# Kernel optimization log

Measured on AMD Instinct MI355X. Metric: run time of the kernel, lower is better.

The kernel has to match this reference:

```python
import jax, jax.numpy as jnp
from jax import lax
import numpy as np

DIM = 256
D_STATE = 16
D_CONV = 4
EXPAND = 2
D_INNER = EXPAND * DIM          # 512
DT_RANK = (DIM + 15) // 16      # 16
EPS = 1e-5


def setup_inputs() -> dict:
    key = jax.random.key(0)
    ks = jax.random.split(key, 8)
    B, H, W = 8, 32, 32
    dt_init = 0.01  # softplus(b_dt) ~= dt_init at init (mamba-style)
    return {
        "x": jax.random.normal(ks[0], (B, DIM, H, W), jnp.float32),
        "ln_gamma": jnp.ones((DIM,), jnp.float32),
        "ln_beta": jnp.zeros((DIM,), jnp.float32),
        "W_in": jax.random.normal(ks[1], (DIM, 2 * D_INNER), jnp.float32) * 0.02,
        "conv_w": jax.random.normal(ks[2], (D_INNER, D_CONV), jnp.float32) * 0.2,
        "conv_b": jnp.zeros((D_INNER,), jnp.float32),
        "W_xproj": jax.random.normal(ks[3], (D_INNER, DT_RANK + 2 * D_STATE), jnp.float32) * 0.02,
        "W_dt": jax.random.normal(ks[4], (DT_RANK, D_INNER), jnp.float32) * 0.05,
        "b_dt": jnp.full((D_INNER,), float(np.log(np.expm1(dt_init))), jnp.float32),
        "A_log": jnp.log(jnp.broadcast_to(
            jnp.arange(1, D_STATE + 1, dtype=jnp.float32), (D_INNER, D_STATE))),
        "D_skip": jnp.ones((D_INNER,), jnp.float32),
        "W_out": jax.random.normal(ks[5], (D_INNER, DIM), jnp.float32) * 0.02,
    }


def _mamba_layer(x, ln_gamma, ln_beta, W_in, conv_w, conv_b, W_xproj,
                 W_dt, b_dt, A_log, D_skip, W_out):
    B, C, H, W = x.shape
    L = H * W
    # (B,C,H,W) -> (B, L, C)
    xf = x.transpose(0, 2, 3, 1).reshape(B, L, C)
    # LayerNorm over channel dim
    mu = xf.mean(-1, keepdims=True)
    var = ((xf - mu) ** 2).mean(-1, keepdims=True)
    xn = (xf - mu) * lax.rsqrt(var + EPS) * ln_gamma + ln_beta
    # in_proj -> u (ssm branch) and z (gate branch)
    xz = xn @ W_in                              # [B, L, 2*D_INNER]
    u, z = xz[..., :D_INNER], xz[..., D_INNER:]
    # causal depthwise conv1d over L, then SiLU
    uc = u.transpose(0, 2, 1)                   # [B, D_INNER, L]
    uc = lax.conv_general_dilated(
        uc, conv_w[:, None, :], window_strides=(1,),
        padding=[(D_CONV - 1, 0)], feature_group_count=D_INNER)
    u2 = jax.nn.silu(uc + conv_b[None, :, None]).transpose(0, 2, 1)  # [B, L, D_INNER]
    # input-dependent dt, B, C
    dbc = u2 @ W_xproj                          # [B, L, DT_RANK + 2*D_STATE]
    dt = jax.nn.softplus(dbc[..., :DT_RANK] @ W_dt + b_dt)            # [B, L, D_INNER]
    Bm = dbc[..., DT_RANK:DT_RANK + D_STATE]    # [B, L, D_STATE]
    Cm = dbc[..., DT_RANK + D_STATE:]           # [B, L, D_STATE]
    A = -jnp.exp(A_log)                         # [D_INNER, D_STATE]

    def step(h, ins):
        dt_t, B_t, C_t, u_t = ins               # [B,Din], [B,S], [B,S], [B,Din]
        dA = jnp.exp(dt_t[:, :, None] * A)      # [B, Din, S]
        h = dA * h + dt_t[:, :, None] * B_t[:, None, :] * u_t[:, :, None]
        y = jnp.einsum('bds,bs->bd', h, C_t)
        return h, y

    h0 = jnp.zeros((B, D_INNER, D_STATE), xf.dtype)
    xs = (dt.transpose(1, 0, 2), Bm.transpose(1, 0, 2),
          Cm.transpose(1, 0, 2), u2.transpose(1, 0, 2))
    _, ys = lax.scan(step, h0, xs)              # ys: [L, B, D_INNER]
    y = ys.transpose(1, 0, 2) + u2 * D_skip     # skip connection D*u
    y = y * jax.nn.silu(z)                      # gate
    o = y @ W_out                               # [B, L, C]
    return o.reshape(B, H, W, C).transpose(0, 3, 1, 2) + x


def reference(x, ln_gamma, ln_beta, W_in, conv_w, conv_b, W_xproj,
              W_dt, b_dt, A_log, D_skip, W_out):
    return _mamba_layer(x, ln_gamma, ln_beta, W_in, conv_w, conv_b, W_xproj,
                        W_dt, b_dt, A_log, D_skip, W_out)
```

## Files before the change

kernel.cpp:

```cpp
#include <hip/hip_runtime.h>
#include <hip/hip_bf16.h>
#include <math.h>

#define DIMC   256
#define DI     512
#define DS     16
#define DTR    16
#define NX     48
#define BATCH  8
#define LSEQ   1024
#define MROWS  8192
#define CHUNK  32
#define NC     (LSEQ / CHUNK)

typedef __attribute__((ext_vector_type(8))) short short8;
typedef __attribute__((ext_vector_type(4))) float f32x4;

__device__ __forceinline__ unsigned short f2bf(float v) {
  __hip_bfloat16 h = __float2bfloat16(v);
  return *reinterpret_cast<unsigned short*>(&h);
}
__device__ __forceinline__ float bf2f(unsigned short u) {
  return __int_as_float(((int)u) << 16);
}

__device__ __forceinline__ void load_lds16(const void* g, void* l) {
  __builtin_amdgcn_global_load_lds(
      (const __attribute__((address_space(1))) unsigned int*)g,
      (__attribute__((address_space(3))) unsigned int*)l, 16, 0, 0);
}

__global__ __launch_bounds__(256) void prologue(const float* __restrict__ W_in,
                                                const float* __restrict__ W_out,
                                                const float* __restrict__ W_xproj,
                                                const float* __restrict__ W_dt,
                                                const float* __restrict__ x,
                                                const float* __restrict__ gamma,
                                                const float* __restrict__ beta,
                                                unsigned short* __restrict__ Wib,
                                                unsigned short* __restrict__ Wob,
                                                unsigned short* __restrict__ Wxpb,
                                                unsigned short* __restrict__ Wdtb,
                                                unsigned short* __restrict__ xnb) {
  __shared__ float sx[DIMC][67];
  __shared__ float smean[64], srs[64];
  const int blk = blockIdx.x, tid = threadIdx.x;
  if (blk < 384) {
    float (*t)[67] = sx;
    const float* W; unsigned short* Wt; int K, N, bx, by;
    if (blk < 256) { W = W_in;  Wt = Wib; K = DIMC; N = 1024; bx = blk & 31; by = blk >> 5; }
    else           { W = W_out; Wt = Wob; K = DI;   N = DIMC; bx = (blk - 256) & 7; by = (blk - 256) >> 3; }
    int n0 = bx * 32, k0 = by * 32;
    int tx = tid & 31, ty = tid >> 5;
    for (int i = ty; i < 32; i += 8) t[i][tx] = W[(size_t)(k0 + i) * N + n0 + tx];
    __syncthreads();
    for (int i = ty; i < 32; i += 8)
      Wt[(size_t)(n0 + i) * K + k0 + tx] = f2bf(t[tx][i]);
    return;
  }
  if (blk < 512) {
    int idx = (blk - 384) * 256 + tid;
    int n = idx >> 9, k = idx & 511;
    Wxpb[idx] = (n < NX) ? f2bf(W_xproj[(size_t)k * NX + n]) : (unsigned short)0;
    return;
  }
  if (blk < 576) {
    int idx = (blk - 512) * 256 + tid;
    int n = idx >> 5, k = idx & 31;
    Wdtb[idx] = (k < DTR) ? f2bf(W_dt[(size_t)k * DI + n]) : (unsigned short)0;
    return;
  }
  const int lb = blk - 576;
  const int b = lb >> 4, l0 = (lb & 15) * 64;
  {
    const int cbase = tid >> 2;
    const int lp = (tid & 3) * 16;
#pragma unroll
    for (int cg = 0; cg < 4; ++cg) {
      const int c = cg * 64 + cbase;
      const float* p = x + ((size_t)b * DIMC + c) * LSEQ + l0 + lp;
#pragma unroll
      for (int q = 0; q < 4; ++q) {
        float4 v = *(const float4*)(p + q * 4);
        sx[c][lp + q * 4 + 0] = v.x;
        sx[c][lp + q * 4 + 1] = v.y;
        sx[c][lp + q * 4 + 2] = v.z;
        sx[c][lp + q * 4 + 3] = v.w;
      }
    }
  }
  __syncthreads();
  {
    const int lane = tid & 63, w = tid >> 6;
    const int l = (w << 4) + (lane & 15);
    const int quad = lane >> 4;
    float sum = 0.f, sq = 0.f;
#pragma unroll 8
    for (int cc = 0; cc < 64; ++cc) {
      float v = sx[quad * 64 + cc][l];
      sum += v; sq += v * v;
    }
    sum += __shfl_xor(sum, 16); sq += __shfl_xor(sq, 16);
    sum += __shfl_xor(sum, 32); sq += __shfl_xor(sq, 32);
    if (quad == 0) {
      float mean = sum * (1.f / 256.f);
      float var  = sq * (1.f / 256.f) - mean * mean;
      smean[l] = mean; srs[l] = rsqrtf(var + 1e-5f);
    }
  }
  __syncthreads();
  {
    const float gg = gamma[tid], bb = beta[tid];
    const size_t base = ((size_t)b * LSEQ + l0) * DIMC + tid;
#pragma unroll 4
    for (int ll = 0; ll < 64; ++ll) {
      float v = (sx[tid][ll] - smean[ll]) * srs[ll] * gg + bb;
      xnb[base + (size_t)ll * DIMC] = f2bf(v);
    }
  }
}

__global__ __launch_bounds__(256) void gemm_bf16_128(const unsigned short* __restrict__ A,
                                                     const unsigned short* __restrict__ Bt,
                                                     unsigned short* __restrict__ Cb,
                                                     int M, int N, int K) {
  __shared__ unsigned short As[128][32];
  __shared__ unsigned short Bs[128][32];
  const int tid = threadIdx.x;
  const int lane = tid & 63, wave = tid >> 6;
  const int wm = wave >> 1, wn = wave & 1;
  const int quad = lane >> 4, l16 = lane & 15;
  const int m0 = blockIdx.y * 128, n0 = blockIdx.x * 128;

  f32x4 acc[4][4];
#pragma unroll
  for (int i = 0; i < 4; ++i)
#pragma unroll
    for (int j = 0; j < 4; ++j) acc[i][j] = (f32x4){0.f, 0.f, 0.f, 0.f};

  for (int k0 = 0; k0 < K; k0 += 32) {
#pragma unroll
    for (int q = 0; q < 2; ++q) {
      int id = q * 256 + tid;
      int row = id >> 2, c = id & 3;
      load_lds16(A + (size_t)(m0 + row) * K + k0 + c * 8,
                 (char*)&As[0][0] + (size_t)(q * 256 + wave * 64) * 16);
    }
#pragma unroll
    for (int q = 0; q < 2; ++q) {
      int id = q * 256 + tid;
      int row = id >> 2, c = id & 3;
      load_lds16(Bt + (size_t)(n0 + row) * K + k0 + c * 8,
                 (char*)&Bs[0][0] + (size_t)(q * 256 + wave * 64) * 16);
    }
    __syncthreads();
    short8 af[4], bfr[4];
#pragma unroll
    for (int i = 0; i < 4; ++i)
      af[i] = *(const short8*)&As[wm * 64 + i * 16 + l16][quad * 8];
#pragma unroll
    for (int j = 0; j < 4; ++j)
      bfr[j] = *(const short8*)&Bs[wn * 64 + j * 16 + l16][quad * 8];
#pragma unroll
    for (int i = 0; i < 4; ++i)
#pragma unroll
      for (int j = 0; j < 4; ++j)
        acc[i][j] = __builtin_amdgcn_mfma_f32_16x16x32_bf16(af[i], bfr[j], acc[i][j], 0, 0, 0);
    __syncthreads();
  }

#pragma unroll
  for (int i = 0; i < 4; ++i) {
    int rowb = wm * 64 + i * 16 + quad * 4;
#pragma unroll
    for (int j = 0; j < 4; ++j) {
      int n = n0 + wn * 64 + j * 16 + l16;
#pragma unroll
      for (int r = 0; r < 4; ++r)
        Cb[(size_t)(m0 + rowb + r) * N + n] = f2bf(acc[i][j][r]);
    }
  }
}

#define GTM 128
#define GTN 64
#define GBK 32
__global__ __launch_bounds__(256) void gemm_bf16(const unsigned short* __restrict__ A,
                                                 const unsigned short* __restrict__ Bt,
                                                 void* __restrict__ Cout,
                                                 int M, int N, int K, int mode,
                                                 const float* __restrict__ X) {
  __shared__ unsigned short As[GTM][GBK];
  __shared__ unsigned short Bs[GTN][GBK];
  const int tid = threadIdx.x;
  const int lane = tid & 63, wave = tid >> 6;
  const int wm = wave >> 1, wn = wave & 1;
  const int quad = lane >> 4, l16 = lane & 15;
  const int m0 = blockIdx.y * GTM, n0 = blockIdx.x * GTN;

  f32x4 acc[4][2];
#pragma unroll
  for (int i = 0; i < 4; ++i)
#pragma unroll
    for (int j = 0; j < 2; ++j) acc[i][j] = (f32x4){0.f, 0.f, 0.f, 0.f};

  for (int k0 = 0; k0 < K; k0 += GBK) {
#pragma unroll
    for (int q = 0; q < 2; ++q) {
      int id = q * 256 + tid;
      int row = id >> 2, c = id & 3;
      load_lds16(A + (size_t)(m0 + row) * K + k0 + c * 8,
                 (char*)&As[0][0] + (size_t)(q * 256 + wave * 64) * 16);
    }
    {
      int row = tid >> 2, c = tid & 3;
      load_lds16(Bt + (size_t)(n0 + row) * K + k0 + c * 8,
                 (char*)&Bs[0][0] + (size_t)(wave * 64) * 16);
    }
    __syncthreads();
    short8 af[4], bfrag[2];
#pragma unroll
    for (int i = 0; i < 4; ++i)
      af[i] = *(const short8*)&As[wm * 64 + i * 16 + l16][quad * 8];
#pragma unroll
    for (int j = 0; j < 2; ++j)
      bfrag[j] = *(const short8*)&Bs[wn * 32 + j * 16 + l16][quad * 8];
#pragma unroll
    for (int i = 0; i < 4; ++i)
#pragma unroll
      for (int j = 0; j < 2; ++j)
        acc[i][j] = __builtin_amdgcn_mfma_f32_16x16x32_bf16(af[i], bfrag[j], acc[i][j], 0, 0, 0);
    __syncthreads();
  }

  if (mode == 2) {
    unsigned short* Cb = (unsigned short*)Cout;
#pragma unroll
    for (int i = 0; i < 4; ++i) {
      int rowb = wm * 64 + i * 16 + quad * 4;
#pragma unroll
      for (int j = 0; j < 2; ++j) {
        int n = n0 + wn * 32 + j * 16 + l16;
#pragma unroll
        for (int r = 0; r < 4; ++r)
          Cb[(size_t)(m0 + rowb + r) * N + n] = f2bf(acc[i][j][r]);
      }
    }
  } else {
    float* C = (float*)Cout;
#pragma unroll
    for (int i = 0; i < 4; ++i) {
      int m = m0 + wm * 64 + i * 16 + quad * 4;
      int b = m >> 10, l = m & 1023;
#pragma unroll
      for (int j = 0; j < 2; ++j) {
        int n = n0 + wn * 32 + j * 16 + l16;
        size_t o = (size_t)b * (DIMC * LSEQ) + (size_t)n * LSEQ + l;
        f32x4 xv = *(const f32x4*)(X + o);
        f32x4 rv = acc[i][j] + xv;
        *(f32x4*)(C + o) = rv;
      }
    }
  }
}

__global__ __launch_bounds__(256) void conv_xproj_dt(
    const unsigned short* __restrict__ xzb,
    const float* __restrict__ conv_w,
    const float* __restrict__ conv_b,
    const unsigned short* __restrict__ Wxpb,
    const unsigned short* __restrict__ Wdtb,
    const float* __restrict__ b_dt,
    float* __restrict__ dbcBC,
    unsigned int* __restrict__ dtu) {
  __shared__ unsigned short sxz[19][512];
  __shared__ unsigned short su[16][512 + 8];
  __shared__ unsigned short sdbc[16][40];
  const int m0 = blockIdx.x * 16;
  const int l0 = m0 & 1023;
  const int tid = threadIdx.x, lane = tid & 63, w = tid >> 6;
  const int quad = lane >> 4, l16 = lane & 15;

#pragma unroll
  for (int q = 0; q < 5; ++q) {
    int id = q * 256 + tid;
    if (id < 19 * 64) {
      int rr = id >> 6, c8 = id & 63;
      uint4 v; v.x = 0u; v.y = 0u; v.z = 0u; v.w = 0u;
      if (l0 - 3 + rr >= 0)
        v = *(const uint4*)(xzb + (size_t)(m0 - 3 + rr) * 1024 + c8 * 8);
      *(uint4*)&sxz[rr][c8 * 8] = v;
    }
  }
  __syncthreads();

#pragma unroll 4
  for (int q = 0; q < 32; ++q) {
    int idx = q * 256 + tid;
    int r = idx >> 9, c = idx & 511;
    float4 wv = *(const float4*)(conv_w + c * 4);
    float acc = conv_b[c];
    acc = fmaf(bf2f(sxz[r + 0][c]), wv.x, acc);
    acc = fmaf(bf2f(sxz[r + 1][c]), wv.y, acc);
    acc = fmaf(bf2f(sxz[r + 2][c]), wv.z, acc);
    acc = fmaf(bf2f(sxz[r + 3][c]), wv.w, acc);
    float u = acc / (1.f + __expf(-acc));
    su[r][c] = f2bf(u);
  }
  __syncthreads();

  f32x4 acc = (f32x4){0.f, 0.f, 0.f, 0.f};
#pragma unroll 4
  for (int k0 = 0; k0 < 512; k0 += 32) {
    short8 af = *(const short8*)&su[l16][k0 + quad * 8];
    short8 bf = *(const short8*)(Wxpb + (size_t)(w * 16 + l16) * 512 + k0 + quad * 8);
    acc = __builtin_amdgcn_mfma_f32_16x16x32_bf16(af, bf, acc, 0, 0, 0);
  }
  if (w == 1 || w == 2) {
#pragma unroll
    for (int r = 0; r < 4; ++r)
      dbcBC[(size_t)(m0 + quad * 4 + r) * 32 + (w - 1) * 16 + l16] = acc[r];
  }
  if (w < 2) {
#pragma unroll
    for (int r = 0; r < 4; ++r)
      sdbc[quad * 4 + r][w * 16 + l16] = f2bf(acc[r]);
  }
  __syncthreads();

  short8 af0 = *(const short8*)&sdbc[l16][quad * 8];
#pragma unroll
  for (int jn = 0; jn < 8; ++jn) {
    const int n0 = w * 128 + jn * 16;
    short8 bf = *(const short8*)(Wdtb + (size_t)(n0 + l16) * 32 + quad * 8);
    f32x4 a0 = (f32x4){0.f, 0.f, 0.f, 0.f};
    a0 = __builtin_amdgcn_mfma_f32_16x16x32_bf16(af0, bf, a0, 0, 0, 0);
    const float bd = b_dt[n0 + l16];
#pragma unroll
    for (int r = 0; r < 4; ++r) {
      int lr0 = quad * 4 + r;
      float v = a0[r] + bd;
      float sp = (v > 20.f) ? v : log1pf(__expf(v));
      unsigned int u0 = (unsigned int)su[lr0][n0 + l16];
      dtu[(size_t)(m0 + lr0) * DI + n0 + l16] = u0 | ((unsigned int)f2bf(sp) << 16);
    }
  }
}

__global__ __launch_bounds__(256) void scan_pass1(const unsigned int* __restrict__ dtu,
                                                  const float* __restrict__ dbcBC,
                                                  const float* __restrict__ A_log,
                                                  float* __restrict__ hend,
                                                  float* __restrict__ Ssum) {
  const int bb = blockIdx.x, dh = blockIdx.y, cc = blockIdx.z;
  const int tid = threadIdx.x;
  const int d = dh * 256 + tid;

  __shared__ float sB[CHUNK][16];
  const size_t mbase = (size_t)bb * LSEQ + cc * CHUNK;
#pragma unroll
  for (int q = 0; q < 2; ++q) {
    int lin = q * 256 + tid;
    int tt = lin >> 4, ss = lin & 15;
    sB[tt][ss] = dbcBC[(mbase + tt) * 32 + ss];
  }

  float Ads[16];
  {
    const f32x4* pa = (const f32x4*)(A_log + (size_t)d * DS);
#pragma unroll
    for (int q = 0; q < 4; ++q) {
      f32x4 v = pa[q];
#pragma unroll
      for (int r = 0; r < 4; ++r) Ads[q * 4 + r] = -__expf(v[r]);
    }
  }
  __syncthreads();

  float h[16];
#pragma unroll
  for (int s = 0; s < 16; ++s) h[s] = 0.f;
  float dts = 0.f;
  const unsigned int* pdu = dtu + mbase * DI + d;
#pragma unroll 4
  for (int tt = 0; tt < CHUNK; ++tt) {
    unsigned int wv = pdu[(size_t)tt * DI];
    float dt = bf2f((unsigned short)(wv >> 16));
    float u  = bf2f((unsigned short)(wv & 0xffff));
    dts += dt;
    float c = dt * u;
#pragma unroll
    for (int s = 0; s < 16; ++s)
      h[s] = fmaf(__expf(dt * Ads[s]), h[s], c * sB[tt][s]);
  }
  const size_t ci = (size_t)(bb * NC + cc) * DI + d;
  f32x4* ph = (f32x4*)(hend + ci * DS);
#pragma unroll
  for (int q = 0; q < 4; ++q) {
    f32x4 v;
#pragma unroll
    for (int r = 0; r < 4; ++r) v[r] = h[q * 4 + r];
    ph[q] = v;
  }
  Ssum[ci] = dts;
}

__global__ __launch_bounds__(256) void scan_pass2(const float* __restrict__ A_log,
                                                  const float* __restrict__ hend,
                                                  const float* __restrict__ Ssum,
                                                  float* __restrict__ hin) {
  const int bb = blockIdx.x, dblk = blockIdx.y;
  const int tid = threadIdx.x;
  const int di = tid >> 4, s = tid & 15;
  const int d = dblk * 16 + di;
  const float Ads = -__expf(A_log[d * DS + s]);
  float h = 0.f;
#pragma unroll 4
  for (int cc = 0; cc < NC; ++cc) {
    size_t ci = ((size_t)(bb * NC + cc) * DI + d);
    hin[ci * DS + s] = h;
    h = fmaf(__expf(Ads * Ssum[ci]), h, hend[ci * DS + s]);
  }
}

__global__ __launch_bounds__(256) void scan_pass3(const unsigned int* __restrict__ dtu,
                                                  const float* __restrict__ dbcBC,
                                                  const unsigned short* __restrict__ xzb,
                                                  const float* __restrict__ A_log,
                                                  const float* __restrict__ D_skip,
                                                  const float* __restrict__ hin,
                                                  unsigned short* __restrict__ yb) {
  const int bb = blockIdx.x, dh = blockIdx.y, cc = blockIdx.z;
  const int tid = threadIdx.x;
  const int d = dh * 256 + tid;

  __shared__ float sB[CHUNK][16];
  __shared__ float sC[CHUNK][16];
  const size_t mbase = (size_t)bb * LSEQ + cc * CHUNK;
#pragma unroll
  for (int q = 0; q < 2; ++q) {
    int lin = q * 256 + tid;
    int tt = lin >> 4, ss = lin & 15;
    sB[tt][ss] = dbcBC[(mbase + tt) * 32 + ss];
    sC[tt][ss] = dbcBC[(mbase + tt) * 32 + 16 + ss];
  }

  float Ads[16];
  {
    const f32x4* pa = (const f32x4*)(A_log + (size_t)d * DS);
#pragma unroll
    for (int q = 0; q < 4; ++q) {
      f32x4 v = pa[q];
#pragma unroll
      for (int r = 0; r < 4; ++r) Ads[q * 4 + r] = -__expf(v[r]);
    }
  }

  float h[16];
  {
    const f32x4* ph = (const f32x4*)(hin + ((size_t)(bb * NC + cc) * DI + d) * DS);
#pragma unroll
    for (int q = 0; q < 4; ++q) {
      f32x4 v = ph[q];
#pragma unroll
      for (int r = 0; r < 4; ++r) h[q * 4 + r] = v[r];
    }
  }
  __syncthreads();

  const float Dsk = D_skip[d];
  const unsigned int* pdu = dtu + mbase * DI + d;
  const unsigned short* pz = xzb + mbase * 1024 + DI + d;
  unsigned short* py = yb + mbase * DI + d;
#pragma unroll 4
  for (int tt = 0; tt < CHUNK; ++tt) {
    unsigned int wv = pdu[(size_t)tt * DI];
    float dt = bf2f((unsigned short)(wv >> 16));
    float u  = bf2f((unsigned short)(wv & 0xffff));
    float c = dt * u;
    float y = u * Dsk;
#pragma unroll
    for (int s = 0; s < 16; ++s) {
      h[s] = fmaf(__expf(dt * Ads[s]), h[s], c * sB[tt][s]);
      y = fmaf(h[s], sC[tt][s], y);
    }
    float z = bf2f(pz[(size_t)tt * 1024]);
    y *= z / (1.f + __expf(-z));
    py[(size_t)tt * DI] = f2bf(y);
  }
}

extern "C" void kernel_launch(void* const* d_in, const int* in_sizes, int n_in,
                              void* d_out, int out_size, void* d_ws, size_t ws_size,
                              hipStream_t stream) {
  const float* x       = (const float*)d_in[0];
  const float* ln_g    = (const float*)d_in[1];
  const float* ln_b    = (const float*)d_in[2];
  const float* W_in    = (const float*)d_in[3];
  const float* conv_w  = (const float*)d_in[4];
  const float* conv_b  = (const float*)d_in[5];
  const float* W_xproj = (const float*)d_in[6];
  const float* W_dt    = (const float*)d_in[7];
  const float* b_dt    = (const float*)d_in[8];
  const float* A_log   = (const float*)d_in[9];
  const float* D_skip  = (const float*)d_in[10];
  const float* W_out   = (const float*)d_in[11];
  float* out = (float*)d_out;

  float* ws    = (float*)d_ws;
  float* dbcBC = ws;
  float* hend  = dbcBC + (size_t)MROWS * 32;
  float* hin   = hend + (size_t)BATCH * NC * DI * DS;
  float* Ssum  = hin  + (size_t)BATCH * NC * DI * DS;
  unsigned int* dtu = (unsigned int*)(Ssum + (size_t)BATCH * NC * DI);
  unsigned short* xzb  = (unsigned short*)(dtu + (size_t)MROWS * DI);
  unsigned short* yb   = xzb + (size_t)MROWS * 1024;
  unsigned short* xnb  = yb;
  unsigned short* Wib  = yb  + (size_t)MROWS * DI;
  unsigned short* Wob  = Wib + (size_t)DIMC * 1024;
  unsigned short* Wxpb = Wob + (size_t)DI * DIMC;
  unsigned short* Wdtb = Wxpb + (size_t)64 * 512;

  prologue<<<704, 256, 0, stream>>>(W_in, W_out, W_xproj, W_dt, x, ln_g, ln_b,
                                    Wib, Wob, Wxpb, Wdtb, xnb);

  gemm_bf16_128<<<dim3(1024 / 128, MROWS / 128), 256, 0, stream>>>(
      xnb, Wib, xzb, MROWS, 1024, DIMC);

  conv_xproj_dt<<<MROWS / 16, 256, 0, stream>>>(xzb, conv_w, conv_b,
                                                Wxpb, Wdtb, b_dt, dbcBC, dtu);

  dim3 gp13(BATCH, 2, NC);
  dim3 gp2(BATCH, DI / 16);
  scan_pass1<<<gp13, 256, 0, stream>>>(dtu, dbcBC, A_log, hend, Ssum);
  scan_pass2<<<gp2, 256, 0, stream>>>(A_log, hend, Ssum, hin);
  scan_pass3<<<gp13, 256, 0, stream>>>(dtu, dbcBC, xzb, A_log, D_skip, hin, yb);

  gemm_bf16<<<dim3(DIMC / GTN, MROWS / GTM), 256, 0, stream>>>(
      yb, Wob, out, MROWS, DIMC, DI, 1, x);
}
```

Measured before the change: 185.9 us.

## Fuse three scan passes into one persistent kernel with grid barriers

Merges the chunked scan's three kernels into a single launch of 512 blocks. Blocks synchronise across the grid with atomic-counter barriers; the counters are reset by the preceding conv kernel. The chunk's dt/u and B/C data are staged once into LDS with async global-to-LDS loads and reused in both the local pass and the output pass, instead of being re-read from global memory. The intent is to remove two launch gaps and the duplicate loads, at the cost of relying on all blocks being co-resident (launch_bounds of 2 blocks per CU) and of spin-wait overhead.

```diff
diff --git a/kernel.cpp b/kernel.cpp
--- a/kernel.cpp
+++ b/kernel.cpp
@@ -28,6 +28,21 @@
   __builtin_amdgcn_global_load_lds(
       (const __attribute__((address_space(1))) unsigned int*)g,
       (__attribute__((address_space(3))) unsigned int*)l, 16, 0, 0);
+}
+
+__device__ __forceinline__ void gridbar(unsigned int* ctr, unsigned int nblk) {
+  __syncthreads();
+  if (threadIdx.x == 0) {
+    __threadfence();
+    __hip_atomic_fetch_add(ctr, 1u, __ATOMIC_ACQ_REL, __HIP_MEMORY_SCOPE_AGENT);
+    for (int it = 0; it < (1 << 20); ++it) {
+      if (__hip_atomic_load(ctr, __ATOMIC_ACQUIRE, __HIP_MEMORY_SCOPE_AGENT) >= nblk)
+        break;
+      __builtin_amdgcn_s_sleep(8);
+    }
+    __threadfence();
+  }
+  __syncthreads();
 }
 
 __global__ __launch_bounds__(256) void prologue(const float* __restrict__ W_in,
@@ -272,7 +287,8 @@
     const unsigned short* __restrict__ Wdtb,
     const float* __restrict__ b_dt,
     float* __restrict__ dbcBC,
-    unsigned int* __restrict__ dtu) {
+    unsigned int* __restrict__ dtu,
+    unsigned int* __restrict__ bar) {
   __shared__ unsigned short sxz[19][512];
   __shared__ unsigned short su[16][512 + 8];
   __shared__ unsigned short sdbc[16][40];
@@ -280,6 +296,8 @@
   const int l0 = m0 & 1023;
   const int tid = threadIdx.x, lane = tid & 63, w = tid >> 6;
   const int quad = lane >> 4, l16 = lane & 15;
+
+  if (blockIdx.x == 0 && tid < 2) bar[tid] = 0u;
 
 #pragma unroll
   for (int q = 0; q < 5; ++q) {
@@ -347,23 +365,36 @@
   }
 }
 
-__global__ __launch_bounds__(256) void scan_pass1(const unsigned int* __restrict__ dtu,
-                                                  const float* __restrict__ dbcBC,
-                                                  const float* __restrict__ A_log,
-                                                  float* __restrict__ hend,
-                                                  float* __restrict__ Ssum) {
+__global__ __launch_bounds__(256, 2) void scan_all(
+    const unsigned int* __restrict__ dtu,
+    const float* __restrict__ dbcBC,
+    const unsigned short* __restrict__ xzb,
+    const float* __restrict__ A_log,
+    const float* __restrict__ D_skip,
+    float* __restrict__ hend,
+    float* __restrict__ Ssum,
+    float* __restrict__ hin,
+    unsigned int* __restrict__ bar,
+    unsigned short* __restrict__ yb) {
   const int bb = blockIdx.x, dh = blockIdx.y, cc = blockIdx.z;
   const int tid = threadIdx.x;
+  const int wave = tid >> 6;
   const int d = dh * 256 + tid;
-
-  __shared__ float sB[CHUNK][16];
+  const unsigned int nblk = gridDim.x * gridDim.y * gridDim.z;
+
+  __shared__ unsigned int sdu[CHUNK][256];
+  __shared__ float sBC[CHUNK][32];
+
   const size_t mbase = (size_t)bb * LSEQ + cc * CHUNK;
-#pragma unroll
-  for (int q = 0; q < 2; ++q) {
-    int lin = q * 256 + tid;
-    int tt = lin >> 4, ss = lin & 15;
-    sB[tt][ss] = dbcBC[(mbase + tt) * 32 + ss];
-  }
+
+#pragma unroll
+  for (int q = 0; q < 8; ++q) {
+    int c = q * 256 + tid;
+    load_lds16(dtu + (mbase + (c >> 6)) * DI + dh * 256 + (c & 63) * 4,
+               (char*)&sdu[0][0] + (size_t)(q * 256 + wave * 64) * 16);
+  }
+  load_lds16(dbcBC + (mbase + (tid >> 3)) * 32 + (tid & 7) * 4,
+             (char*)&sBC[0][0] + (size_t)(wave * 64) * 16);
 
   float Ads[16];
   {
@@ -381,84 +412,59 @@
 #pragma unroll
   for (int s = 0; s < 16; ++s) h[s] = 0.f;
   float dts = 0.f;
-  const unsigned int* pdu = dtu + mbase * DI + d;
 #pragma unroll 4
   for (int tt = 0; tt < CHUNK; ++tt) {
-    unsigned int wv = pdu[(size_t)tt * DI];
+    unsigned int wv = sdu[tt][tid];
     float dt = bf2f((unsigned short)(wv >> 16));
     float u  = bf2f((unsigned short)(wv & 0xffff));
     dts += dt;
-    float c = dt * u;
-#pragma unroll
-    for (int s = 0; s < 16; ++s)
-      h[s] = fmaf(__expf(dt * Ads[s]), h[s], c * sB[tt][s]);
+    float cdu = dt * u;
+    f32x4 B0 = *(const f32x4*)&sBC[tt][0];
+    f32x4 B1 = *(const f32x4*)&sBC[tt][4];
+    f32x4 B2 = *(const f32x4*)&sBC[tt][8];
+    f32x4 B3 = *(const f32x4*)&sBC[tt][12];
+#pragma unroll
+    for (int r = 0; r < 4; ++r) h[r]      = fmaf(__expf(dt * Ads[r]),      h[r],      cdu * B0[r]);
+#pragma unroll
+    for (int r = 0; r < 4; ++r) h[4 + r]  = fmaf(__expf(dt * Ads[4 + r]),  h[4 + r],  cdu * B1[r]);
+#pragma unroll
+    for (int r = 0; r < 4; ++r) h[8 + r]  = fmaf(__expf(dt * Ads[8 + r]),  h[8 + r],  cdu * B2[r]);
+#pragma unroll
+    for (int r = 0; r < 4; ++r) h[12 + r] = fmaf(__expf(dt * Ads[12 + r]), h[12 + r], cdu * B3[r]);
   }
   const size_t ci = (size_t)(bb * NC + cc) * DI + d;
-  f32x4* ph = (f32x4*)(hend + ci * DS);
-#pragma unroll
-  for (int q = 0; q < 4; ++q) {
-    f32x4 v;
-#pragma unroll
-    for (int r = 0; r < 4; ++r) v[r] = h[q * 4 + r];
-    ph[q] = v;
-  }
-  Ssum[ci] = dts;
-}
-
-__global__ __launch_bounds__(256) void scan_pass2(const float* __restrict__ A_log,
-                                                  const float* __restrict__ hend,
-                                                  const float* __restrict__ Ssum,
-                                                  float* __restrict__ hin) {
-  const int bb = blockIdx.x, dblk = blockIdx.y;
-  const int tid = threadIdx.x;
-  const int di = tid >> 4, s = tid & 15;
-  const int d = dblk * 16 + di;
-  const float Ads = -__expf(A_log[d * DS + s]);
-  float h = 0.f;
+  {
+    f32x4* ph = (f32x4*)(hend + ci * DS);
+#pragma unroll
+    for (int q = 0; q < 4; ++q) {
+      f32x4 v;
+#pragma unroll
+      for (int r = 0; r < 4; ++r) v[r] = h[q * 4 + r];
+      ph[q] = v;
+    }
+    Ssum[ci] = dts;
+  }
+
+  gridbar(bar + 0, nblk);
+
+  if (cc < 16) {
+    const int dblk = dh * 16 + cc;
+    const int di = tid >> 4, s2 = tid & 15;
+    const int dd = dblk * 16 + di;
+    const float A2 = -__expf(A_log[dd * DS + s2]);
+    float hh = 0.f;
 #pragma unroll 4
-  for (int cc = 0; cc < NC; ++cc) {
-    size_t ci = ((size_t)(bb * NC + cc) * DI + d);
-    hin[ci * DS + s] = h;
-    h = fmaf(__expf(Ads * Ssum[ci]), h, hend[ci * DS + s]);
-  }
-}
-
-__global__ __launch_bounds__(256) void scan_pass3(const unsigned int* __restrict__ dtu,
-                                                  const float* __restrict__ dbcBC,
-                                                  const unsigned short* __restrict__ xzb,
-                                                  const float* __restrict__ A_log,
-                                                  const float* __restrict__ D_skip,
-                                                  const float* __restrict__ hin,
-                                                  unsigned short* __restrict__ yb) {
-  const int bb = blockIdx.x, dh = blockIdx.y, cc = blockIdx.z;
-  const int tid = threadIdx.x;
-  const int d = dh * 256 + tid;
-
-  __shared__ float sB[CHUNK][16];
-  __shared__ float sC[CHUNK][16];
-  const size_t mbase = (size_t)bb * LSEQ + cc * CHUNK;
-#pragma unroll
-  for (int q = 0; q < 2; ++q) {
-    int lin = q * 256 + tid;
-    int tt = lin >> 4, ss = lin & 15;
-    sB[tt][ss] = dbcBC[(mbase + tt) * 32 + ss];
-    sC[tt][ss] = dbcBC[(mbase + tt) * 32 + 16 + ss];
-  }
-
-  float Ads[16];
+    for (int j = 0; j < NC; ++j) {
+      size_t cj = (size_t)(bb * NC + j) * DI + dd;
+      hin[cj * DS + s2] = hh;
+      hh = fmaf(__expf(A2 * Ssum[cj]), hh, hend[cj * DS + s2]);
+    }
+  }
+
+  gridbar(bar + 1, nblk);
+
   {
-    const f32x4* pa = (const f32x4*)(A_log + (size_t)d * DS);
-#pragma unroll
-    for (int q = 0; q < 4; ++q) {
-      f32x4 v = pa[q];
-#pragma unroll
-      for (int r = 0; r < 4; ++r) Ads[q * 4 + r] = -__expf(v[r]);
-    }
-  }
-
-  float h[16];
-  {
-    const f32x4* ph = (const f32x4*)(hin + ((size_t)(bb * NC + cc) * DI + d) * DS);
+    const f32x4* ph = (const f32x4*)(hin + ci * DS);
 #pragma unroll
     for (int q = 0; q < 4; ++q) {
       f32x4 v = ph[q];
@@ -466,24 +472,32 @@
       for (int r = 0; r < 4; ++r) h[q * 4 + r] = v[r];
     }
   }
-  __syncthreads();
-
   const float Dsk = D_skip[d];
-  const unsigned int* pdu = dtu + mbase * DI + d;
   const unsigned short* pz = xzb + mbase * 1024 + DI + d;
   unsigned short* py = yb + mbase * DI + d;
 #pragma unroll 4
   for (int tt = 0; tt < CHUNK; ++tt) {
-    unsigned int wv = pdu[(size_t)tt * DI];
+    unsigned int wv = sdu[tt][tid];
     float dt = bf2f((unsigned short)(wv >> 16));
     float u  = bf2f((unsigned short)(wv & 0xffff));
-    float c = dt * u;
+    float cdu = dt * u;
     float y = u * Dsk;
-#pragma unroll
-    for (int s = 0; s < 16; ++s) {
-      h[s] = fmaf(__expf(dt * Ads[s]), h[s], c * sB[tt][s]);
-      y = fmaf(h[s], sC[tt][s], y);
-    }
+    f32x4 B0 = *(const f32x4*)&sBC[tt][0];
+    f32x4 B1 = *(const f32x4*)&sBC[tt][4];
+    f32x4 B2 = *(const f32x4*)&sBC[tt][8];
+    f32x4 B3 = *(const f32x4*)&sBC[tt][12];
+    f32x4 C0 = *(const f32x4*)&sBC[tt][16];
+    f32x4 C1 = *(const f32x4*)&sBC[tt][20];
+    f32x4 C2 = *(const f32x4*)&sBC[tt][24];
+    f32x4 C3 = *(const f32x4*)&sBC[tt][28];
+#pragma unroll
+    for (int r = 0; r < 4; ++r) { h[r]      = fmaf(__expf(dt * Ads[r]),      h[r],      cdu * B0[r]); y = fmaf(h[r],      C0[r], y); }
+#pragma unroll
+    for (int r = 0; r < 4; ++r) { h[4 + r]  = fmaf(__expf(dt * Ads[4 + r]),  h[4 + r],  cdu * B1[r]); y = fmaf(h[4 + r],  C1[r], y); }
+#pragma unroll
+    for (int r = 0; r < 4; ++r) { h[8 + r]  = fmaf(__expf(dt * Ads[8 + r]),  h[8 + r],  cdu * B2[r]); y = fmaf(h[8 + r],  C2[r], y); }
+#pragma unroll
+    for (int r = 0; r < 4; ++r) { h[12 + r] = fmaf(__expf(dt * Ads[12 + r]), h[12 + r], cdu * B3[r]); y = fmaf(h[12 + r], C3[r], y); }
     float z = bf2f(pz[(size_t)tt * 1024]);
     y *= z / (1.f + __expf(-z));
     py[(size_t)tt * DI] = f2bf(y);
@@ -520,6 +534,7 @@
   unsigned short* Wob  = Wib + (size_t)DIMC * 1024;
   unsigned short* Wxpb = Wob + (size_t)DI * DIMC;
   unsigned short* Wdtb = Wxpb + (size_t)64 * 512;
+  unsigned int*   bar  = (unsigned int*)(Wdtb + (size_t)512 * 32);
 
   prologue<<<704, 256, 0, stream>>>(W_in, W_out, W_xproj, W_dt, x, ln_g, ln_b,
                                     Wib, Wob, Wxpb, Wdtb, xnb);
@@ -528,13 +543,10 @@
       xnb, Wib, xzb, MROWS, 1024, DIMC);
 
   conv_xproj_dt<<<MROWS / 16, 256, 0, stream>>>(xzb, conv_w, conv_b,
-                                                Wxpb, Wdtb, b_dt, dbcBC, dtu);
-
-  dim3 gp13(BATCH, 2, NC);
-  dim3 gp2(BATCH, DI / 16);
-  scan_pass1<<<gp13, 256, 0, stream>>>(dtu, dbcBC, A_log, hend, Ssum);
-  scan_pass2<<<gp2, 256, 0, stream>>>(A_log, hend, Ssum, hin);
-  scan_pass3<<<gp13, 256, 0, stream>>>(dtu, dbcBC, xzb, A_log, D_skip, hin, yb);
+                                                Wxpb, Wdtb, b_dt, dbcBC, dtu, bar);
+
+  scan_all<<<dim3(BATCH, 2, NC), 256, 0, stream>>>(
+      dtu, dbcBC, xzb, A_log, D_skip, hend, Ssum, hin, bar, yb);
 
   gemm_bf16<<<dim3(DIMC / GTN, MROWS / GTM), 256, 0, stream>>>(
       yb, Wob, out, MROWS, DIMC, DI, 1, x);
```

Measured after the change: 321.6 us. +73.0%, slower.

## Fuse chunk-carry scan into pass1 via last-block atomic counter

Applied to the files above, without the earlier changes.

Removes the separate scan_pass2 launch. Each pass1 block now increments a per-(batch, half) atomic counter, and the last block to arrive runs the sequential carry propagation across all chunks to write hin. The counter is reset inside conv_xproj_dt. The x_proj MFMA loop is also split into two independent accumulators to shorten the dependency chain. The trade-off is that a single block per group does the serial 32-chunk carry loop at the tail, and correctness depends on fences and ordering.

```diff
diff --git a/kernel.cpp b/kernel.cpp
--- a/kernel.cpp
+++ b/kernel.cpp
@@ -272,7 +272,8 @@
     const unsigned short* __restrict__ Wdtb,
     const float* __restrict__ b_dt,
     float* __restrict__ dbcBC,
-    unsigned int* __restrict__ dtu) {
+    unsigned int* __restrict__ dtu,
+    unsigned int* __restrict__ cnt) {
   __shared__ unsigned short sxz[19][512];
   __shared__ unsigned short su[16][512 + 8];
   __shared__ unsigned short sdbc[16][40];
@@ -280,6 +281,8 @@
   const int l0 = m0 & 1023;
   const int tid = threadIdx.x, lane = tid & 63, w = tid >> 6;
   const int quad = lane >> 4, l16 = lane & 15;
+
+  if (blockIdx.x == 0 && tid < 16) cnt[tid] = 0u;
 
 #pragma unroll
   for (int q = 0; q < 5; ++q) {
@@ -309,13 +312,18 @@
   }
   __syncthreads();
 
-  f32x4 acc = (f32x4){0.f, 0.f, 0.f, 0.f};
+  f32x4 acc0 = (f32x4){0.f, 0.f, 0.f, 0.f};
+  f32x4 acc1 = (f32x4){0.f, 0.f, 0.f, 0.f};
 #pragma unroll 4
-  for (int k0 = 0; k0 < 512; k0 += 32) {
-    short8 af = *(const short8*)&su[l16][k0 + quad * 8];
-    short8 bf = *(const short8*)(Wxpb + (size_t)(w * 16 + l16) * 512 + k0 + quad * 8);
-    acc = __builtin_amdgcn_mfma_f32_16x16x32_bf16(af, bf, acc, 0, 0, 0);
-  }
+  for (int k0 = 0; k0 < 256; k0 += 32) {
+    short8 afA = *(const short8*)&su[l16][k0 + quad * 8];
+    short8 bfA = *(const short8*)(Wxpb + (size_t)(w * 16 + l16) * 512 + k0 + quad * 8);
+    acc0 = __builtin_amdgcn_mfma_f32_16x16x32_bf16(afA, bfA, acc0, 0, 0, 0);
+    short8 afB = *(const short8*)&su[l16][256 + k0 + quad * 8];
+    short8 bfB = *(const short8*)(Wxpb + (size_t)(w * 16 + l16) * 512 + 256 + k0 + quad * 8);
+    acc1 = __builtin_amdgcn_mfma_f32_16x16x32_bf16(afB, bfB, acc1, 0, 0, 0);
+  }
+  f32x4 acc = acc0 + acc1;
   if (w == 1 || w == 2) {
 #pragma unroll
     for (int r = 0; r < 4; ++r)
@@ -351,12 +359,15 @@
                                                   const float* __restrict__ dbcBC,
                                                   const float* __restrict__ A_log,
                                                   float* __restrict__ hend,
-                                                  float* __restrict__ Ssum) {
+                                                  float* __restrict__ Ssum,
+                                                  float* __restrict__ hin,
+                                                  unsigned int* __restrict__ cnt) {
   const int bb = blockIdx.x, dh = blockIdx.y, cc = blockIdx.z;
   const int tid = threadIdx.x;
   const int d = dh * 256 + tid;
 
   __shared__ float sB[CHUNK][16];
+  __shared__ int sFin;
   const size_t mbase = (size_t)bb * LSEQ + cc * CHUNK;
 #pragma unroll
   for (int q = 0; q < 2; ++q) {
@@ -394,32 +405,51 @@
       h[s] = fmaf(__expf(dt * Ads[s]), h[s], c * sB[tt][s]);
   }
   const size_t ci = (size_t)(bb * NC + cc) * DI + d;
-  f32x4* ph = (f32x4*)(hend + ci * DS);
-#pragma unroll
-  for (int q = 0; q < 4; ++q) {
-    f32x4 v;
-#pragma unroll
-    for (int r = 0; r < 4; ++r) v[r] = h[q * 4 + r];
-    ph[q] = v;
-  }
-  Ssum[ci] = dts;
-}
-
-__global__ __launch_bounds__(256) void scan_pass2(const float* __restrict__ A_log,
-                                                  const float* __restrict__ hend,
-                                                  const float* __restrict__ Ssum,
-                                                  float* __restrict__ hin) {
-  const int bb = blockIdx.x, dblk = blockIdx.y;
-  const int tid = threadIdx.x;
-  const int di = tid >> 4, s = tid & 15;
-  const int d = dblk * 16 + di;
-  const float Ads = -__expf(A_log[d * DS + s]);
-  float h = 0.f;
-#pragma unroll 4
-  for (int cc = 0; cc < NC; ++cc) {
-    size_t ci = ((size_t)(bb * NC + cc) * DI + d);
-    hin[ci * DS + s] = h;
-    h = fmaf(__expf(Ads * Ssum[ci]), h, hend[ci * DS + s]);
+  {
+    f32x4* ph = (f32x4*)(hend + ci * DS);
+#pragma unroll
+    for (int q = 0; q < 4; ++q) {
+      f32x4 v;
+#pragma unroll
+      for (int r = 0; r < 4; ++r) v[r] = h[q * 4 + r];
+      ph[q] = v;
+    }
+    Ssum[ci] = dts;
+  }
+
+  __syncthreads();
+  if (tid == 0) {
+    unsigned int old = __hip_atomic_fetch_add(&cnt[bb * 2 + dh], 1u,
+                                              __ATOMIC_ACQ_REL,
+                                              __HIP_MEMORY_SCOPE_AGENT);
+    sFin = (old == NC - 1) ? 1 : 0;
+  }
+  __syncthreads();
+  if (sFin) {
+    __threadfence();
+    float hh[16];
+#pragma unroll
+    for (int s = 0; s < 16; ++s) hh[s] = 0.f;
+    for (int j = 0; j < NC; ++j) {
+      const size_t cj = (size_t)(bb * NC + j) * DI + d;
+      f32x4* po = (f32x4*)(hin + cj * DS);
+#pragma unroll
+      for (int q = 0; q < 4; ++q) {
+        f32x4 v;
+#pragma unroll
+        for (int r = 0; r < 4; ++r) v[r] = hh[q * 4 + r];
+        po[q] = v;
+      }
+      const float Sj = Ssum[cj];
+      const f32x4* pe = (const f32x4*)(hend + cj * DS);
+#pragma unroll
+      for (int q = 0; q < 4; ++q) {
+        f32x4 e = pe[q];
+#pragma unroll
+        for (int r = 0; r < 4; ++r)
+          hh[q * 4 + r] = fmaf(__expf(Ads[q * 4 + r] * Sj), hh[q * 4 + r], e[r]);
+      }
+    }
   }
 }
 
@@ -520,6 +550,7 @@
   unsigned short* Wob  = Wib + (size_t)DIMC * 1024;
   unsigned short* Wxpb = Wob + (size_t)DI * DIMC;
   unsigned short* Wdtb = Wxpb + (size_t)64 * 512;
+  unsigned int*   cnt  = (unsigned int*)(Wdtb + (size_t)512 * 32);
 
   prologue<<<704, 256, 0, stream>>>(W_in, W_out, W_xproj, W_dt, x, ln_g, ln_b,
                                     Wib, Wob, Wxpb, Wdtb, xnb);
@@ -528,12 +559,10 @@
       xnb, Wib, xzb, MROWS, 1024, DIMC);
 
   conv_xproj_dt<<<MROWS / 16, 256, 0, stream>>>(xzb, conv_w, conv_b,
-                                                Wxpb, Wdtb, b_dt, dbcBC, dtu);
+                                                Wxpb, Wdtb, b_dt, dbcBC, dtu, cnt);
 
   dim3 gp13(BATCH, 2, NC);
-  dim3 gp2(BATCH, DI / 16);
-  scan_pass1<<<gp13, 256, 0, stream>>>(dtu, dbcBC, A_log, hend, Ssum);
-  scan_pass2<<<gp2, 256, 0, stream>>>(A_log, hend, Ssum, hin);
+  scan_pass1<<<gp13, 256, 0, stream>>>(dtu, dbcBC, A_log, hend, Ssum, hin, cnt);
   scan_pass3<<<gp13, 256, 0, stream>>>(dtu, dbcBC, xzb, A_log, D_skip, hin, yb);
 
   gemm_bf16<<<dim3(DIMC / GTN, MROWS / GTM), 256, 0, stream>>>(
```

Result: slower. 224.9 us (+21.0%).
